# Kernel optimization log

Hardware: AMD Instinct MI355X
Metric: run time of the kernel (lower is better)

The kernel has to match this reference:

```python
import jax, jax.numpy as jnp
import numpy as np
import itertools

# Per-group attribute cardinalities (product = number of prototypes per group)
GROUP_DIMS = {
    "gender": [2],
    "hair": [5, 3],
    "top": [8, 5],
    "pants": [8, 5],
    "shoes": [6, 4],
}
TAU = 0.07  # softmax temperature for prototype similarity
B, D = 32768, 512


def _affinity(dims):
    # Faithful to _build_group_affinity: A[i,j] = fraction of matching sub-attribute values
    combos = np.array(list(itertools.product(*[range(d) for d in dims])), dtype=np.int32)  # [K, n_attrs]
    mat = (combos[:, None, :] == combos[None, :, :]).mean(-1).astype(np.float32)  # [K, K]
    return jnp.asarray(mat)


def _l2(v):
    return v / (jnp.linalg.norm(v, axis=-1, keepdims=True) + 1e-6)


def setup_inputs() -> dict:
    key = jax.random.key(0)
    ks = jax.random.split(key, 1 + len(GROUP_DIMS))
    inp = {"x": jax.random.normal(ks[0], (B, D), dtype=jnp.float32)}
    for k, (name, dims) in zip(ks[1:], GROUP_DIMS.items()):
        K = int(np.prod(dims))
        # matches nn.Parameter(torch.randn(K, D) * 0.01)
        inp[f"P_{name}"] = jax.random.normal(k, (K, D), dtype=jnp.float32) * 0.01
    return inp


def reference(x, P_gender, P_hair, P_top, P_pants, P_shoes):
    protos = {"gender": P_gender, "hair": P_hair, "top": P_top, "pants": P_pants, "shoes": P_shoes}
    xn = _l2(x)  # [B, D]
    outs = []
    for name, P in protos.items():
        A = _affinity(GROUP_DIMS[name])          # [K, K] constant affinity buffer
        logits = (xn @ _l2(P).T) / TAU           # [B, K] cosine-similarity prototype lookup
        q = jax.nn.softmax(logits, axis=-1)      # soft assignment
        q_aff = q @ A                            # affinity-weighted assignment
        q_aff = q_aff / (q_aff.sum(-1, keepdims=True) + 1e-6)
        outs.append(q_aff @ P)                   # [B, D] affinity-smoothed quantized feature
    return jnp.stack(outs, axis=1)               # [B, n_groups, D]
```

## Files before the change

kernel.cpp:

```cpp
#include <hip/hip_runtime.h>
#include <hip/hip_bf16.h>
#include <math.h>


constexpr int D    = 512;
constexpr int KTOT = 121;
constexpr float TAU = 0.07f;

constexpr int GB[5]  = {0, 2, 17, 57, 97};
constexpr int GK[5]  = {2, 15, 40, 40, 24};
constexpr int GD2[5] = {1, 3, 5, 5, 4};
constexpr int GNA[5] = {1, 2, 2, 2, 2};
constexpr int KS0[5] = {0, 0, 0, 1, 3};
constexpr int KS1[5] = {1, 1, 2, 4, 4};

using f32x4 = __attribute__((ext_vector_type(4))) float;
using s16x8 = __attribute__((ext_vector_type(8))) short;

__device__ __forceinline__ const float* pick(int k,
    const float* P0, const float* P1, const float* P2, const float* P3, const float* P4,
    int* kl) {
  if (k < 2)  { *kl = k;      return P0; }
  if (k < 17) { *kl = k - 2;  return P1; }
  if (k < 57) { *kl = k - 17; return P2; }
  if (k < 97) { *kl = k - 57; return P3; }
  *kl = k - 97; return P4;
}

__device__ __forceinline__ short f2bf(float f) {
  __hip_bfloat16 h = __float2bfloat16(f);
  return *reinterpret_cast<short*>(&h);
}

__global__ __launch_bounds__(256) void prep_all(
    const float* __restrict__ P0, const float* __restrict__ P1,
    const float* __restrict__ P2, const float* __restrict__ P3,
    const float* __restrict__ P4, unsigned short* __restrict__ pnbf,
    unsigned short* __restrict__ mptbf) {
  const int tid = threadIdx.x;
  if (blockIdx.x < 8) {
    const int ct = blockIdx.x;
    __shared__ float lsum[16][17];
    __shared__ float linv[16];
    {
      const int i = tid >> 4, part = tid & 15;
      const int col = ct * 16 + i;
      float s = 0.f;
      if (col < KTOT) {
        int kl; const float* P = pick(col, P0, P1, P2, P3, P4, &kl);
        const float* row = P + (size_t)kl * D + part * 32;
        #pragma unroll
        for (int e = 0; e < 32; ++e) { float v = row[e]; s += v * v; }
      }
      lsum[i][part] = s;
    }
    __syncthreads();
    if (tid < 16) {
      float s = 0.f;
      #pragma unroll
      for (int p = 0; p < 16; ++p) s += lsum[tid][p];
      linv[tid] = 1.f / (sqrtf(s) + 1e-6f);
    }
    __syncthreads();
    for (int s = 0; s < 16; ++s) {
      #pragma unroll
      for (int half = 0; half < 2; ++half) {
        const int e = tid + half * 256;
        const int lane = e >> 3, j = e & 7;
        const int col = ct * 16 + (lane & 15);
        const int k   = s * 32 + (lane >> 4) * 8 + j;
        float v = 0.f;
        if (col < KTOT) {
          int kl; const float* P = pick(col, P0, P1, P2, P3, P4, &kl);
          v = P[(size_t)kl * D + k] * linv[lane & 15];
        }
        pnbf[(size_t)(ct * 16 + s) * 512 + e] = (unsigned short)f2bf(v);
      }
    }
  } else {
    const int c2 = blockIdx.x - 8;
    const int c = c2 >> 2, ks = c2 & 3;
    #pragma unroll
    for (int half = 0; half < 2; ++half) {
      const int e = tid + half * 256;
      const int lane = e >> 3, j = e & 7;
      const int gd = c * 16 + (lane & 15);
      const int k  = ks * 32 + (lane >> 4) * 8 + j;
      const int g = gd >> 9, d = gd & (D - 1);
      float v = 0.f;
      if (k >= GB[g] && k < GB[g] + GK[g]) {
        int kl = k - GB[g];
        const float* P = (g == 0) ? P0 : (g == 1) ? P1 : (g == 2) ? P2 : (g == 3) ? P3 : P4;
        int d2 = GD2[g], na = GNA[g], K = GK[g];
        int a1 = kl / d2, a2 = kl % d2;
        float s = 0.f, m = 0.f;
        for (int jj = 0; jj < K; jj++) {
          float aff;
          if (na == 1) {
            aff = (jj == kl) ? 1.f : 0.f;
          } else {
            int b1 = jj / d2, b2 = jj % d2;
            aff = 0.5f * (float)((a1 == b1) + (a2 == b2));
          }
          s += aff;
          m += aff * P[(size_t)jj * D + d];
        }
        v = m / (s + 1e-6f);
      }
      mptbf[(size_t)c2 * 512 + e] = (unsigned short)f2bf(v);
    }
  }
}

template <int G>
__device__ __forceinline__ void phase2_group(
    const s16x8 (&af2)[4], const unsigned short* __restrict__ mptbf,
    float* __restrict__ ob, float* __restrict__ obase, int ch, int lane) {
  const int l15 = lane & 15, hi = lane >> 4;
  #pragma unroll 1
  for (int i = 0; i < 4; ++i) {
    const int s = G * 8 + i * 2 + ch;
    const unsigned short* bp = mptbf + (size_t)(s * 4) * 4 * 512 + lane * 8;
    f32x4 a0 = (f32x4){0.f, 0.f, 0.f, 0.f}, a1 = a0, a2 = a0, a3 = a0;
    #pragma unroll
    for (int ks = KS0[G]; ks < KS1[G]; ++ks) {
      s16x8 b0 = *(const s16x8*)(bp + (0 * 4 + ks) * 512);
      s16x8 b1 = *(const s16x8*)(bp + (1 * 4 + ks) * 512);
      s16x8 b2 = *(const s16x8*)(bp + (2 * 4 + ks) * 512);
      s16x8 b3 = *(const s16x8*)(bp + (3 * 4 + ks) * 512);
      a0 = __builtin_amdgcn_mfma_f32_16x16x32_bf16(b0, af2[ks], a0, 0, 0, 0);
      a1 = __builtin_amdgcn_mfma_f32_16x16x32_bf16(b1, af2[ks], a1, 0, 0, 0);
      a2 = __builtin_amdgcn_mfma_f32_16x16x32_bf16(b2, af2[ks], a2, 0, 0, 0);
      a3 = __builtin_amdgcn_mfma_f32_16x16x32_bf16(b3, af2[ks], a3, 0, 0, 0);
    }
    *(f32x4*)&ob[l15 * 68 +  0 + hi * 4] = a0;
    *(f32x4*)&ob[l15 * 68 + 16 + hi * 4] = a1;
    *(f32x4*)&ob[l15 * 68 + 32 + hi * 4] = a2;
    *(f32x4*)&ob[l15 * 68 + 48 + hi * 4] = a3;
    float* gp = obase + (size_t)s * 64 + l15 * 4;
    #pragma unroll
    for (int i2 = 0; i2 < 4; ++i2) {
      const int row = i2 * 4 + hi;
      f32x4 v = *(const f32x4*)&ob[row * 68 + l15 * 4];
      __builtin_nontemporal_store(v, (f32x4*)(gp + (size_t)row * (5 * D)));
    }
  }
}

__global__ __launch_bounds__(256, 4) void fused_main(
    const float* __restrict__ x, const unsigned short* __restrict__ pnbf,
    const unsigned short* __restrict__ mptbf, float* __restrict__ out) {
  __shared__ __align__(16) float smem[4352];
  __shared__ float xsqs[32];
  float (*lred)[33] = (float (*)[33])smem;

  const int tid  = threadIdx.x;
  const int lane = tid & 63;
  const int w    = __builtin_amdgcn_readfirstlane(tid >> 6);
  const int r0   = blockIdx.x * 32;

  const int wr = (w & 1) << 4;
  const int ch = w >> 1;
  const int ko = (lane >> 4) << 3;

  {
    const int arow = wr + (lane & 15);
    const float* xrow = x + (size_t)(r0 + arow) * D + ko;

    f32x4 acc[4];
    #pragma unroll
    for (int t = 0; t < 4; ++t) acc[t] = (f32x4){0.f, 0.f, 0.f, 0.f};
    float xsq = 0.f;

    #pragma unroll 4
    for (int s = 0; s < 16; ++s) {
      float4 a0 = *(const float4*)(xrow + s * 32);
      float4 a1 = *(const float4*)(xrow + s * 32 + 4);
      xsq += a0.x * a0.x + a0.y * a0.y + a0.z * a0.z + a0.w * a0.w
           + a1.x * a1.x + a1.y * a1.y + a1.z * a1.z + a1.w * a1.w;
      s16x8 af;
      af[0] = f2bf(a0.x); af[1] = f2bf(a0.y); af[2] = f2bf(a0.z); af[3] = f2bf(a0.w);
      af[4] = f2bf(a1.x); af[5] = f2bf(a1.y); af[6] = f2bf(a1.z); af[7] = f2bf(a1.w);
      #pragma unroll
      for (int t = 0; t < 4; ++t) {
        s16x8 bfv = *(const s16x8*)(pnbf + (size_t)(((ch << 2) + t) * 16 + s) * 512 + lane * 8);
        acc[t] = __builtin_amdgcn_mfma_f32_16x16x32_bf16(af, bfv, acc[t], 0, 0, 0);
      }
    }

    xsq += __shfl_xor(xsq, 16);
    xsq += __shfl_xor(xsq, 32);
    if (ch == 0 && lane < 16) xsqs[wr + lane] = xsq;

    const int drow = wr + ((lane >> 4) << 2);
    #pragma unroll
    for (int t = 0; t < 4; ++t) {
      const int col = (ch << 6) + (t << 4) + (lane & 15);
      #pragma unroll
      for (int j = 0; j < 4; ++j) lred[col][drow + j] = acc[t][j];
    }
  }
  __syncthreads();

  if (lane < 32) {
    const float scale = 1.f / ((sqrtf(xsqs[lane]) + 1e-6f) * TAU);
    const int gfirst = (w == 0) ? 0 : w;
    const int glast  = (w == 0) ? 4 : w;
    for (int g = gfirst; g <= glast; g += (w == 0) ? 4 : 1) {
      float mx = -1e30f;
      for (int kk = 0; kk < GK[g]; ++kk)
        mx = fmaxf(mx, lred[GB[g] + kk][lane]);
      float E = 0.f;
      for (int kk = 0; kk < GK[g]; ++kk) {
        float e = __expf((lred[GB[g] + kk][lane] - mx) * scale);
        lred[GB[g] + kk][lane] = e;
        E += e;
      }
      const float inv = 1.f / E;
      for (int kk = 0; kk < GK[g]; ++kk) lred[GB[g] + kk][lane] *= inv;
    }
  }
  __syncthreads();

  s16x8 af2[4];
  {
    const int ar = wr + (lane & 15);
    #pragma unroll
    for (int s = 0; s < 4; ++s) {
      const int kbase = s * 32 + ko;
      s16x8 f;
      #pragma unroll
      for (int j = 0; j < 8; ++j) f[j] = f2bf(lred[kbase + j][ar]);
      af2[s] = f;
    }
  }
  __syncthreads();

  {
    float* ob    = smem + w * (16 * 68);
    float* obase = out + (size_t)(r0 + wr) * (5 * D);

    phase2_group<0>(af2, mptbf, ob, obase, ch, lane);
    phase2_group<1>(af2, mptbf, ob, obase, ch, lane);
    phase2_group<2>(af2, mptbf, ob, obase, ch, lane);
    phase2_group<3>(af2, mptbf, ob, obase, ch, lane);
    phase2_group<4>(af2, mptbf, ob, obase, ch, lane);
  }
}

extern "C" void kernel_launch(void* const* d_in, const int* in_sizes, int n_in,
                              void* d_out, int out_size, void* d_ws, size_t ws_size,
                              hipStream_t stream) {
  const float* x  = (const float*)d_in[0];
  const float* P0 = (const float*)d_in[1];
  const float* P1 = (const float*)d_in[2];
  const float* P2 = (const float*)d_in[3];
  const float* P3 = (const float*)d_in[4];
  const float* P4 = (const float*)d_in[5];
  float* out = (float*)d_out;

  unsigned short* pnbf  = (unsigned short*)d_ws;
  unsigned short* mptbf = pnbf + 128 * 512;

  prep_all<<<dim3(648), dim3(256), 0, stream>>>(P0, P1, P2, P3, P4, pnbf, mptbf);
  fused_main<<<dim3(1024), dim3(256), 0, stream>>>(x, pnbf, mptbf, out);
}
```

Baseline: 116.0 us.

## Stage full 512-wide output rows in LDS and sweep-store them block-wide

Phase 2 now has the two waves sharing a row slab write their MFMA results into a shared 16x512 LDS buffer. The whole block then stores full contiguous 2 KB rows to global memory, replacing per-wave 64-column stores, and the nontemporal hint is dropped. The aim is more coalesced, longer write bursts for the large output. In exchange, half the waves sit idle during each fill, two block barriers are added per subround (20 in total), and LDS use roughly doubles, which may lower occupancy.

```diff
diff --git a/kernel.cpp b/kernel.cpp
--- a/kernel.cpp
+++ b/kernel.cpp
@@ -13,6 +13,8 @@
 constexpr int GNA[5] = {1, 2, 2, 2, 2};
 constexpr int KS0[5] = {0, 0, 0, 1, 3};
 constexpr int KS1[5] = {1, 1, 2, 4, 4};
+
+constexpr int BSTRIDE = 516;
 
 using f32x4 = __attribute__((ext_vector_type(4))) float;
 using s16x8 = __attribute__((ext_vector_type(8))) short;
@@ -113,13 +115,14 @@
 }
 
 template <int G>
-__device__ __forceinline__ void phase2_group(
+__device__ __forceinline__ void phase2_fill(
     const s16x8 (&af2)[4], const unsigned short* __restrict__ mptbf,
-    float* __restrict__ ob, float* __restrict__ obase, int ch, int lane) {
+    float* __restrict__ buf, int ch, int lane) {
   const int l15 = lane & 15, hi = lane >> 4;
   #pragma unroll 1
   for (int i = 0; i < 4; ++i) {
-    const int s = G * 8 + i * 2 + ch;
+    const int sloc = i * 2 + ch;
+    const int s    = G * 8 + sloc;
     const unsigned short* bp = mptbf + (size_t)(s * 4) * 4 * 512 + lane * 8;
     f32x4 a0 = (f32x4){0.f, 0.f, 0.f, 0.f}, a1 = a0, a2 = a0, a3 = a0;
     #pragma unroll
@@ -133,24 +136,29 @@
       a2 = __builtin_amdgcn_mfma_f32_16x16x32_bf16(b2, af2[ks], a2, 0, 0, 0);
       a3 = __builtin_amdgcn_mfma_f32_16x16x32_bf16(b3, af2[ks], a3, 0, 0, 0);
     }
-    *(f32x4*)&ob[l15 * 68 +  0 + hi * 4] = a0;
-    *(f32x4*)&ob[l15 * 68 + 16 + hi * 4] = a1;
-    *(f32x4*)&ob[l15 * 68 + 32 + hi * 4] = a2;
-    *(f32x4*)&ob[l15 * 68 + 48 + hi * 4] = a3;
-    float* gp = obase + (size_t)s * 64 + l15 * 4;
-    #pragma unroll
-    for (int i2 = 0; i2 < 4; ++i2) {
-      const int row = i2 * 4 + hi;
-      f32x4 v = *(const f32x4*)&ob[row * 68 + l15 * 4];
-      __builtin_nontemporal_store(v, (f32x4*)(gp + (size_t)row * (5 * D)));
-    }
+    float* bb = buf + l15 * BSTRIDE + sloc * 64 + hi * 4;
+    *(f32x4*)(bb +  0) = a0;
+    *(f32x4*)(bb + 16) = a1;
+    *(f32x4*)(bb + 32) = a2;
+    *(f32x4*)(bb + 48) = a3;
+  }
+}
+
+__device__ __forceinline__ void sweep_store(
+    const float* __restrict__ buf, float* __restrict__ gb,
+    int swrow, int swcol) {
+  #pragma unroll
+  for (int it = 0; it < 8; ++it) {
+    const int row = it * 2 + swrow;
+    f32x4 v = *(const f32x4*)(buf + row * BSTRIDE + swcol);
+    *(f32x4*)(gb + (size_t)row * 2560 + swcol) = v;
   }
 }
 
 __global__ __launch_bounds__(256, 4) void fused_main(
     const float* __restrict__ x, const unsigned short* __restrict__ pnbf,
     const unsigned short* __restrict__ mptbf, float* __restrict__ out) {
-  __shared__ __align__(16) float smem[4352];
+  __shared__ __align__(16) float smem[8256];
   __shared__ float xsqs[32];
   float (*lred)[33] = (float (*)[33])smem;
 
@@ -237,14 +245,20 @@
   __syncthreads();
 
   {
-    float* ob    = smem + w * (16 * 68);
-    float* obase = out + (size_t)(r0 + wr) * (5 * D);
-
-    phase2_group<0>(af2, mptbf, ob, obase, ch, lane);
-    phase2_group<1>(af2, mptbf, ob, obase, ch, lane);
-    phase2_group<2>(af2, mptbf, ob, obase, ch, lane);
-    phase2_group<3>(af2, mptbf, ob, obase, ch, lane);
-    phase2_group<4>(af2, mptbf, ob, obase, ch, lane);
+    float* buf = smem;
+    const int swrow = tid >> 7;
+    const int swcol = (tid & 127) * 4;
+
+#define SUBROUND(SLAB2, G)                                                    \
+    if ((w & 1) == (SLAB2)) phase2_fill<G>(af2, mptbf, buf, ch, lane);        \
+    __syncthreads();                                                          \
+    sweep_store(buf, out + (size_t)(r0 + (SLAB2) * 16) * 2560 + (G) * 512,    \
+                swrow, swcol);                                                \
+    __syncthreads();
+
+    SUBROUND(0, 0) SUBROUND(0, 1) SUBROUND(0, 2) SUBROUND(0, 3) SUBROUND(0, 4)
+    SUBROUND(1, 0) SUBROUND(1, 1) SUBROUND(1, 2) SUBROUND(1, 3) SUBROUND(1, 4)
+#undef SUBROUND
   }
 }
 
```

Measured after the change: 123.1 us. 6.1% more time.
